# Kernel optimization log

Measured on AMD Instinct MI355X. Metric: run time of the kernel, lower is better.

The kernel has to match this reference:

```python
import jax, jax.numpy as jnp
import numpy as np

ROUTING_ROUNDS = 3
EPS = 1e-9

def squash(s, axis):
    # s * ||s||^2 / (1 + ||s||^2) / ||s||
    sn = jnp.sum(s * s, axis=axis, keepdims=True)
    return s * (sn / (1.0 + sn)) * jax.lax.rsqrt(sn + EPS)

def setup_inputs() -> dict:
    key = jax.random.key(0)
    k1, k2 = jax.random.split(key)
    B, N, D = 32, 2048, 32   # batch, input caps num, input caps dim
    C, V = 64, 32            # output caps num, output caps dim
    input_layer = jax.random.normal(k1, (B, N, D), dtype=jnp.float32)
    W = 0.1 * jax.random.normal(k2, (1, N, C, V, D), dtype=jnp.float32)
    return {"input_layer": input_layer, "W": W}

def reference(input_layer, W):
    # input_layer: [B, N, D]; W: [1, N, C, V, D]
    B, N, D = input_layer.shape
    Wn = W[0]  # [N, C, V, D]
    C, V = Wn.shape[1], Wn.shape[2]
    # caps_predicted (u_hat): [B, N, C, V]  (== tf matmul of W_tiled @ caps_output_tiled, squeezed)
    u_hat = jnp.einsum('bnd,ncvd->bncv', input_layer, Wn)
    b = jnp.zeros((B, N, C), dtype=input_layer.dtype)
    v = None
    for _ in range(ROUTING_ROUNDS):
        r = jax.nn.softmax(b, axis=2)                      # [B, N, C]
        s = jnp.einsum('bnc,bncv->bcv', r, u_hat)          # weighted_sum over input caps
        v = squash(s, axis=-1)                             # [B, C, V]
        # agreement = u_hat^T . v : [B, N, C]
        b = b + jnp.einsum('bncv,bcv->bnc', u_hat, v)
    # match original output shape [B, 1, caps_num, vec_len, 1]
    return v[:, None, :, :, None]
```

## Files before the change

### kernel.cpp

```cpp
#include <hip/hip_runtime.h>
#include <hip/hip_bf16.h>


#define B_ 32
#define N_ 2048
#define D_ 32
#define C_ 64
#define V_ 32

typedef __attribute__((ext_vector_type(4))) float f32x4;
typedef __attribute__((ext_vector_type(4))) int i32x4;
typedef __attribute__((ext_vector_type(2))) int i32x2;
typedef __bf16 bf16x8 __attribute__((ext_vector_type(8)));

__device__ __forceinline__ unsigned f2bf1(float f) {
  unsigned u = __builtin_bit_cast(unsigned, f);
  return (u + 0x7FFFu + ((u >> 16) & 1u)) >> 16;
}
__device__ __forceinline__ float bf2f(unsigned h) {
  unsigned u = h << 16;
  return __builtin_bit_cast(float, u);
}

__device__ __forceinline__ bf16x8 cvt_frag(f32x4 lo, f32x4 hi) {
  i32x4 r;
  r[0] = f2bf1(lo[0]) | (f2bf1(lo[1]) << 16);
  r[1] = f2bf1(lo[2]) | (f2bf1(lo[3]) << 16);
  r[2] = f2bf1(hi[0]) | (f2bf1(hi[1]) << 16);
  r[3] = f2bf1(hi[2]) | (f2bf1(hi[3]) << 16);
  return __builtin_bit_cast(bf16x8, r);
}

__global__ __launch_bounds__(256) void uhat_kernel(const float* __restrict__ x,
                                                   const float* __restrict__ W,
                                                   unsigned short* __restrict__ uh) {
  const int n = blockIdx.x;
  const int wave = threadIdx.x >> 6;
  const int l = threadIdx.x & 63;
  const int l16 = l & 15, kg = l >> 4;

  bf16x8 xb[2];
#pragma unroll
  for (int bt = 0; bt < 2; ++bt) {
    const float* xp = x + (((size_t)(bt * 16 + l16)) * N_ + n) * D_ + kg * 8;
    xb[bt] = cvt_frag(*(const f32x4*)xp, *(const f32x4*)(xp + 4));
  }
  const f32x4 zero = {0.f, 0.f, 0.f, 0.f};
  const float* wbase = W + ((size_t)n * 2048 + wave * 512 + l16) * D_ + kg * 8;
  unsigned short* ubase = uh + (size_t)n * 65536 + (size_t)(wave * 512 + kg * 4);

  f32x4 wl[2][2];
  {
    const float* w0 = wbase;
    const float* w1 = wbase + (size_t)16 * D_;
    wl[0][0] = *(const f32x4*)w0; wl[0][1] = *(const f32x4*)(w0 + 4);
    wl[1][0] = *(const f32x4*)w1; wl[1][1] = *(const f32x4*)(w1 + 4);
  }
#pragma unroll
  for (int pt = 0; pt < 32; ++pt) {
    f32x4 c0 = wl[pt & 1][0], c1 = wl[pt & 1][1];
    if (pt < 30) {
      const float* wp = wbase + (size_t)((pt + 2) * 16) * D_;
      wl[pt & 1][0] = *(const f32x4*)wp;
      wl[pt & 1][1] = *(const f32x4*)(wp + 4);
    }
    bf16x8 wfrag = cvt_frag(c0, c1);
#pragma unroll
    for (int bt = 0; bt < 2; ++bt) {
      f32x4 acc = __builtin_amdgcn_mfma_f32_16x16x32_bf16(wfrag, xb[bt], zero, 0, 0, 0);
      i32x2 dv;
      dv[0] = (int)(f2bf1(acc[0]) | (f2bf1(acc[1]) << 16));
      dv[1] = (int)(f2bf1(acc[2]) | (f2bf1(acc[3]) << 16));
      *(i32x2*)(ubase + (size_t)(bt * 16 + l16) * 2048 + pt * 16) = dv;
    }
  }
}

template <int ROUND>
__global__ __launch_bounds__(256) void routing_kernel(const unsigned short* __restrict__ uh,
                                                      const float* __restrict__ vsum,
                                                      float* __restrict__ part) {
  const int b = blockIdx.x >> 5;
  const int chunk = blockIdx.x & 31;
  const int wave = threadIdx.x >> 6;
  const int l = threadIdx.x & 63;

  float vs[32];
  if (ROUND >= 2) {
    const f32x4* vp = (const f32x4*)(vsum + ((size_t)b * 64 + l) * 32);
#pragma unroll
    for (int i = 0; i < 8; ++i) {
      f32x4 t = vp[i];
      vs[4 * i] = t[0]; vs[4 * i + 1] = t[1]; vs[4 * i + 2] = t[2]; vs[4 * i + 3] = t[3];
    }
  }
  float sacc[32];
#pragma unroll
  for (int v = 0; v < 32; ++v) sacc[v] = 0.f;

  const int n0 = chunk * 64 + wave * 16;
  for (int ni = 0; ni < 16; ++ni) {
    const int n = n0 + ni;
    const i32x4* up = (const i32x4*)(uh + ((size_t)n * 32 + b) * 2048 + l * 32);
    i32x4 qs0 = up[0], qs1 = up[1], qs2 = up[2], qs3 = up[3];
    float u[32];
#pragma unroll
    for (int i = 0; i < 4; ++i) {
      unsigned v0 = (unsigned)qs0[i], v1 = (unsigned)qs1[i], v2 = (unsigned)qs2[i], v3 = (unsigned)qs3[i];
      u[0 + 2 * i] = bf2f(v0 & 0xffffu);  u[0 + 2 * i + 1] = bf2f(v0 >> 16);
      u[8 + 2 * i] = bf2f(v1 & 0xffffu);  u[8 + 2 * i + 1] = bf2f(v1 >> 16);
      u[16 + 2 * i] = bf2f(v2 & 0xffffu); u[16 + 2 * i + 1] = bf2f(v2 >> 16);
      u[24 + 2 * i] = bf2f(v3 & 0xffffu); u[24 + 2 * i + 1] = bf2f(v3 >> 16);
    }
    float r;
    if (ROUND >= 2) {
      float br = 0.f;
#pragma unroll
      for (int v = 0; v < 32; ++v) br = fmaf(u[v], vs[v], br);
      float m = br;
#pragma unroll
      for (int off = 32; off; off >>= 1) m = fmaxf(m, __shfl_xor(m, off, 64));
      float e = __expf(br - m);
      float den = e;
#pragma unroll
      for (int off = 32; off; off >>= 1) den += __shfl_xor(den, off, 64);
      r = e / den;
    } else {
      r = 1.0f / 64.0f;
    }
#pragma unroll
    for (int v = 0; v < 32; ++v) sacc[v] = fmaf(r, u[v], sacc[v]);
  }

  __shared__ float red[4][64][33];
#pragma unroll
  for (int v = 0; v < 32; ++v) red[wave][l][v] = sacc[v];
  __syncthreads();
  const int t = threadIdx.x;
  f32x4 o0, o1;
#pragma unroll
  for (int i = 0; i < 4; ++i) {
    const int e0 = t * 8 + i, e1 = t * 8 + 4 + i;
    o0[i] = red[0][e0 >> 5][e0 & 31] + red[1][e0 >> 5][e0 & 31] +
            red[2][e0 >> 5][e0 & 31] + red[3][e0 >> 5][e0 & 31];
    o1[i] = red[0][e1 >> 5][e1 & 31] + red[1][e1 >> 5][e1 & 31] +
            red[2][e1 >> 5][e1 & 31] + red[3][e1 >> 5][e1 & 31];
  }
  float* pp = part + ((size_t)blockIdx.x) * 2048 + t * 8;
  *(f32x4*)pp = o0;
  *(f32x4*)(pp + 4) = o1;
}

template <int ROUND>
__global__ __launch_bounds__(256) void squash_kernel(const float* __restrict__ part,
                                                     float* __restrict__ vsum,
                                                     float* __restrict__ out) {
  const int t = blockIdx.x * 256 + threadIdx.x;
  const int b = t >> 11;
  const int e = t & 2047;
  float sv = 0.f;
#pragma unroll
  for (int k = 0; k < 32; ++k) sv += part[((size_t)(b * 32 + k)) * 2048 + e];
  float sq = sv * sv;
#pragma unroll
  for (int off = 16; off; off >>= 1) sq += __shfl_xor(sq, off, 64);
  float scale = (sq / (1.f + sq)) * rsqrtf(sq + 1e-9f);
  float val = sv * scale;
  out[t] = val;
  if (ROUND == 1) vsum[t] = val;
  else if (ROUND == 2) vsum[t] += val;
}

extern "C" void kernel_launch(void* const* d_in, const int* in_sizes, int n_in,
                              void* d_out, int out_size, void* d_ws, size_t ws_size,
                              hipStream_t stream) {
  const float* x = (const float*)d_in[0];
  const float* W = (const float*)d_in[1];
  float* out = (float*)d_out;

  const size_t UH_BYTES = (size_t)B_ * N_ * C_ * V_ * 2;
  const size_t PART_BYTES = (size_t)B_ * 32 * 2048 * 4;
  const size_t VSUM_BYTES = (size_t)B_ * C_ * V_ * 4;
  if (ws_size < UH_BYTES + PART_BYTES + VSUM_BYTES) return;

  unsigned short* uh = (unsigned short*)d_ws;
  float* part = (float*)((char*)d_ws + UH_BYTES);
  float* vsum = (float*)((char*)d_ws + UH_BYTES + PART_BYTES);

  uhat_kernel<<<N_, 256, 0, stream>>>(x, W, uh);
  routing_kernel<1><<<B_ * 32, 256, 0, stream>>>(uh, vsum, part);
  squash_kernel<1><<<256, 256, 0, stream>>>(part, vsum, out);
  routing_kernel<2><<<B_ * 32, 256, 0, stream>>>(uh, vsum, part);
  squash_kernel<2><<<256, 256, 0, stream>>>(part, vsum, out);
  routing_kernel<3><<<B_ * 32, 256, 0, stream>>>(uh, vsum, part);
  squash_kernel<3><<<256, 256, 0, stream>>>(part, vsum, out);
}
```

Baseline: 342.9 us.

## Reorder u_hat layout via LDS staging and remap routing blocks to batch pairs

The uhat kernel now stages each group of 8 MFMA output tiles in per-wave LDS and writes u_hat with full 16-byte coalesced stores in a new layout. The layout interleaves batch rows at 16-element granularity inside each n and c-pair. Routing blocks now cover two batches with 32 n each per wave, which halves the grid and changes the partial-sum indexing, and squash is updated to match. The aim is to replace the scattered 8-byte stores in uhat with coalesced ones and to give routing better load locality, at the cost of extra LDS traffic and fewer routing blocks.

```diff
diff --git a/kernel.cpp b/kernel.cpp
--- a/kernel.cpp
+++ b/kernel.cpp
@@ -39,6 +39,9 @@
   const int l = threadIdx.x & 63;
   const int l16 = l & 15, kg = l >> 4;
 
+  __shared__ unsigned short lds[4][8 * 640];
+  unsigned short* wlds = lds[wave];
+
   bf16x8 xb[2];
 #pragma unroll
   for (int bt = 0; bt < 2; ++bt) {
@@ -47,7 +50,7 @@
   }
   const f32x4 zero = {0.f, 0.f, 0.f, 0.f};
   const float* wbase = W + ((size_t)n * 2048 + wave * 512 + l16) * D_ + kg * 8;
-  unsigned short* ubase = uh + (size_t)n * 65536 + (size_t)(wave * 512 + kg * 4);
+  unsigned short* ubase = uh + (((size_t)n * 128 + wave * 32) * 512) + l * 8;
 
   f32x4 wl[2][2];
   {
@@ -56,23 +59,39 @@
     wl[0][0] = *(const f32x4*)w0; wl[0][1] = *(const f32x4*)(w0 + 4);
     wl[1][0] = *(const f32x4*)w1; wl[1][1] = *(const f32x4*)(w1 + 4);
   }
-#pragma unroll
-  for (int pt = 0; pt < 32; ++pt) {
-    f32x4 c0 = wl[pt & 1][0], c1 = wl[pt & 1][1];
-    if (pt < 30) {
-      const float* wp = wbase + (size_t)((pt + 2) * 16) * D_;
-      wl[pt & 1][0] = *(const f32x4*)wp;
-      wl[pt & 1][1] = *(const f32x4*)(wp + 4);
-    }
-    bf16x8 wfrag = cvt_frag(c0, c1);
-#pragma unroll
-    for (int bt = 0; bt < 2; ++bt) {
-      f32x4 acc = __builtin_amdgcn_mfma_f32_16x16x32_bf16(wfrag, xb[bt], zero, 0, 0, 0);
-      i32x2 dv;
-      dv[0] = (int)(f2bf1(acc[0]) | (f2bf1(acc[1]) << 16));
-      dv[1] = (int)(f2bf1(acc[2]) | (f2bf1(acc[3]) << 16));
-      *(i32x2*)(ubase + (size_t)(bt * 16 + l16) * 2048 + pt * 16) = dv;
-    }
+
+#pragma unroll
+  for (int g = 0; g < 4; ++g) {
+#pragma unroll
+    for (int pq = 0; pq < 8; ++pq) {
+      const int pt = g * 8 + pq;
+      f32x4 c0 = wl[pt & 1][0], c1 = wl[pt & 1][1];
+      if (pt < 30) {
+        const float* wp = wbase + (size_t)((pt + 2) * 16) * D_;
+        wl[pt & 1][0] = *(const f32x4*)wp;
+        wl[pt & 1][1] = *(const f32x4*)(wp + 4);
+      }
+      bf16x8 wfrag = cvt_frag(c0, c1);
+#pragma unroll
+      for (int bt = 0; bt < 2; ++bt) {
+        f32x4 acc = __builtin_amdgcn_mfma_f32_16x16x32_bf16(wfrag, xb[bt], zero, 0, 0, 0);
+        i32x2 dv;
+        dv[0] = (int)(f2bf1(acc[0]) | (f2bf1(acc[1]) << 16));
+        dv[1] = (int)(f2bf1(acc[2]) | (f2bf1(acc[3]) << 16));
+        *(i32x2*)(wlds + pq * 640 + (bt * 16 + l16) * 20 + kg * 4) = dv;
+      }
+    }
+    __builtin_amdgcn_sched_barrier(0);
+#pragma unroll
+    for (int k = 0; k < 8; ++k) {
+      const unsigned short* src = wlds + k * 640 + (l >> 1) * 20 + (l & 1) * 8;
+      i32x2 lo = *(const i32x2*)src;
+      i32x2 hi = *(const i32x2*)(src + 4);
+      i32x4 vv;
+      vv[0] = lo[0]; vv[1] = lo[1]; vv[2] = hi[0]; vv[3] = hi[1];
+      *(i32x4*)(ubase + ((size_t)(g * 8 + k)) * 512) = vv;
+    }
+    __builtin_amdgcn_sched_barrier(0);
   }
 }
 
@@ -80,10 +99,12 @@
 __global__ __launch_bounds__(256) void routing_kernel(const unsigned short* __restrict__ uh,
                                                       const float* __restrict__ vsum,
                                                       float* __restrict__ part) {
-  const int b = blockIdx.x >> 5;
+  const int pair = blockIdx.x >> 5;
   const int chunk = blockIdx.x & 31;
-  const int wave = threadIdx.x >> 6;
+  const int w = threadIdx.x >> 6;
   const int l = threadIdx.x & 63;
+  const int b = pair * 2 + (w >> 1);
+  const int n0 = chunk * 64 + (w & 1) * 32;
 
   float vs[32];
   if (ROUND >= 2) {
@@ -98,11 +119,13 @@
 #pragma unroll
   for (int v = 0; v < 32; ++v) sacc[v] = 0.f;
 
-  const int n0 = chunk * 64 + wave * 16;
-  for (int ni = 0; ni < 16; ++ni) {
+  for (int ni = 0; ni < 32; ++ni) {
     const int n = n0 + ni;
-    const i32x4* up = (const i32x4*)(uh + ((size_t)n * 32 + b) * 2048 + l * 32);
-    i32x4 qs0 = up[0], qs1 = up[1], qs2 = up[2], qs3 = up[3];
+    const unsigned short* up = uh + (((size_t)n * 128 + 2 * l) * 32 + b) * 16;
+    i32x4 qs0 = *(const i32x4*)up;
+    i32x4 qs1 = *(const i32x4*)(up + 8);
+    i32x4 qs2 = *(const i32x4*)(up + 512);
+    i32x4 qs3 = *(const i32x4*)(up + 520);
     float u[32];
 #pragma unroll
     for (int i = 0; i < 4; ++i) {
@@ -134,21 +157,24 @@
 
   __shared__ float red[4][64][33];
 #pragma unroll
-  for (int v = 0; v < 32; ++v) red[wave][l][v] = sacc[v];
+  for (int v = 0; v < 32; ++v) red[w][l][v] = sacc[v];
   __syncthreads();
   const int t = threadIdx.x;
-  f32x4 o0, o1;
+  f32x4 o0, o1, p0, p1;
 #pragma unroll
   for (int i = 0; i < 4; ++i) {
     const int e0 = t * 8 + i, e1 = t * 8 + 4 + i;
-    o0[i] = red[0][e0 >> 5][e0 & 31] + red[1][e0 >> 5][e0 & 31] +
-            red[2][e0 >> 5][e0 & 31] + red[3][e0 >> 5][e0 & 31];
-    o1[i] = red[0][e1 >> 5][e1 & 31] + red[1][e1 >> 5][e1 & 31] +
-            red[2][e1 >> 5][e1 & 31] + red[3][e1 >> 5][e1 & 31];
-  }
-  float* pp = part + ((size_t)blockIdx.x) * 2048 + t * 8;
-  *(f32x4*)pp = o0;
-  *(f32x4*)(pp + 4) = o1;
+    o0[i] = red[0][e0 >> 5][e0 & 31] + red[1][e0 >> 5][e0 & 31];
+    o1[i] = red[0][e1 >> 5][e1 & 31] + red[1][e1 >> 5][e1 & 31];
+    p0[i] = red[2][e0 >> 5][e0 & 31] + red[3][e0 >> 5][e0 & 31];
+    p1[i] = red[2][e1 >> 5][e1 & 31] + red[3][e1 >> 5][e1 & 31];
+  }
+  float* pp0 = part + ((size_t)blockIdx.x * 2) * 2048 + t * 8;
+  float* pp1 = part + ((size_t)blockIdx.x * 2 + 1) * 2048 + t * 8;
+  *(f32x4*)pp0 = o0;
+  *(f32x4*)(pp0 + 4) = o1;
+  *(f32x4*)pp1 = p0;
+  *(f32x4*)(pp1 + 4) = p1;
 }
 
 template <int ROUND>
@@ -158,9 +184,11 @@
   const int t = blockIdx.x * 256 + threadIdx.x;
   const int b = t >> 11;
   const int e = t & 2047;
+  const int pr = b >> 1, b01 = b & 1;
   float sv = 0.f;
 #pragma unroll
-  for (int k = 0; k < 32; ++k) sv += part[((size_t)(b * 32 + k)) * 2048 + e];
+  for (int k = 0; k < 32; ++k)
+    sv += part[(((size_t)(pr * 32 + k)) * 2 + b01) * 2048 + e];
   float sq = sv * sv;
 #pragma unroll
   for (int off = 16; off; off >>= 1) sq += __shfl_xor(sq, off, 64);
@@ -179,7 +207,7 @@
   float* out = (float*)d_out;
 
   const size_t UH_BYTES = (size_t)B_ * N_ * C_ * V_ * 2;
-  const size_t PART_BYTES = (size_t)B_ * 32 * 2048 * 4;
+  const size_t PART_BYTES = (size_t)512 * 2 * 2048 * 4;
   const size_t VSUM_BYTES = (size_t)B_ * C_ * V_ * 4;
   if (ws_size < UH_BYTES + PART_BYTES + VSUM_BYTES) return;
 
@@ -188,10 +216,10 @@
   float* vsum = (float*)((char*)d_ws + UH_BYTES + PART_BYTES);
 
   uhat_kernel<<<N_, 256, 0, stream>>>(x, W, uh);
-  routing_kernel<1><<<B_ * 32, 256, 0, stream>>>(uh, vsum, part);
+  routing_kernel<1><<<512, 256, 0, stream>>>(uh, vsum, part);
   squash_kernel<1><<<256, 256, 0, stream>>>(part, vsum, out);
-  routing_kernel<2><<<B_ * 32, 256, 0, stream>>>(uh, vsum, part);
+  routing_kernel<2><<<512, 256, 0, stream>>>(uh, vsum, part);
   squash_kernel<2><<<256, 256, 0, stream>>>(part, vsum, out);
-  routing_kernel<3><<<B_ * 32, 256, 0, stream>>>(uh, vsum, part);
+  routing_kernel<3><<<512, 256, 0, stream>>>(uh, vsum, part);
   squash_kernel<3><<<256, 256, 0, stream>>>(part, vsum, out);
 }
```

Result: slower. 426.4 us (+24.3%).

## Stream W through swizzled LDS double buffer via global_load_lds in uhat kernel

Applied to the files above, without the earlier changes.

The uhat kernel now loads W tiles with direct global-to-LDS loads into a per-wave double buffer, using an XOR swizzle so that LDS reads avoid bank conflicts. Loads for the next phase are issued before the current phase computes, with explicit vmcnt waits. The goal is fuller, more coalesced W streaming, and less register pressure than the earlier register prefetch. The costs are 32 KB of LDS per block, which may cut occupancy, and hand-written waitcnt counts that also count the uh stores, so the synchronisation is fragile.

```diff
diff --git a/kernel.cpp b/kernel.cpp
--- a/kernel.cpp
+++ b/kernel.cpp
@@ -31,6 +31,12 @@
   return __builtin_bit_cast(bf16x8, r);
 }
 
+__device__ __forceinline__ void gload16(const float* g, float* l) {
+  __builtin_amdgcn_global_load_lds(
+      (const __attribute__((address_space(1))) void*)g,
+      (__attribute__((address_space(3))) void*)l, 16, 0, 0);
+}
+
 __global__ __launch_bounds__(256) void uhat_kernel(const float* __restrict__ x,
                                                    const float* __restrict__ W,
                                                    unsigned short* __restrict__ uh) {
@@ -38,6 +44,11 @@
   const int wave = threadIdx.x >> 6;
   const int l = threadIdx.x & 63;
   const int l16 = l & 15, kg = l >> 4;
+  const int lrow = l >> 3, lcol = l & 7;
+
+  __shared__ float lds[4][2][1024];
+  float* wbuf0 = &lds[wave][0][0];
+  float* wbuf1 = &lds[wave][1][0];
 
   bf16x8 xb[2];
 #pragma unroll
@@ -45,33 +56,53 @@
     const float* xp = x + (((size_t)(bt * 16 + l16)) * N_ + n) * D_ + kg * 8;
     xb[bt] = cvt_frag(*(const f32x4*)xp, *(const f32x4*)(xp + 4));
   }
+  __builtin_amdgcn_sched_barrier(0);
+
   const f32x4 zero = {0.f, 0.f, 0.f, 0.f};
-  const float* wbase = W + ((size_t)n * 2048 + wave * 512 + l16) * D_ + kg * 8;
+  const int src_off_f = lrow * 32 + ((((lcol * 16) ^ (lrow << 4))) >> 2);
+  const float* wsrc = W + (size_t)n * 65536 + (size_t)wave * 16384 + src_off_f;
   unsigned short* ubase = uh + (size_t)n * 65536 + (size_t)(wave * 512 + kg * 4);
-
-  f32x4 wl[2][2];
-  {
-    const float* w0 = wbase;
-    const float* w1 = wbase + (size_t)16 * D_;
-    wl[0][0] = *(const f32x4*)w0; wl[0][1] = *(const f32x4*)(w0 + 4);
-    wl[1][0] = *(const f32x4*)w1; wl[1][1] = *(const f32x4*)(w1 + 4);
-  }
-#pragma unroll
-  for (int pt = 0; pt < 32; ++pt) {
-    f32x4 c0 = wl[pt & 1][0], c1 = wl[pt & 1][1];
-    if (pt < 30) {
-      const float* wp = wbase + (size_t)((pt + 2) * 16) * D_;
-      wl[pt & 1][0] = *(const f32x4*)wp;
-      wl[pt & 1][1] = *(const f32x4*)(wp + 4);
-    }
-    bf16x8 wfrag = cvt_frag(c0, c1);
-#pragma unroll
-    for (int bt = 0; bt < 2; ++bt) {
-      f32x4 acc = __builtin_amdgcn_mfma_f32_16x16x32_bf16(wfrag, xb[bt], zero, 0, 0, 0);
-      i32x2 dv;
-      dv[0] = (int)(f2bf1(acc[0]) | (f2bf1(acc[1]) << 16));
-      dv[1] = (int)(f2bf1(acc[2]) | (f2bf1(acc[3]) << 16));
-      *(i32x2*)(ubase + (size_t)(bt * 16 + l16) * 2048 + pt * 16) = dv;
+  const unsigned char* rb0 = (const unsigned char*)wbuf0;
+  const unsigned char* rb1 = (const unsigned char*)wbuf1;
+  const int a_base = (kg * 32) ^ ((l16 & 7) << 4);
+
+#pragma unroll
+  for (int sub = 0; sub < 4; ++sub)
+    gload16(wsrc + sub * 256, wbuf0 + sub * 256);
+
+#pragma unroll
+  for (int ph = 0; ph < 16; ++ph) {
+    if (ph < 15) {
+      const float* ws = wsrc + (size_t)(ph + 1) * 1024;
+      float* dbuf = ((ph + 1) & 1) ? wbuf1 : wbuf0;
+#pragma unroll
+      for (int sub = 0; sub < 4; ++sub)
+        gload16(ws + sub * 256, dbuf + sub * 256);
+    }
+    if (ph == 0) {
+      asm volatile("s_waitcnt vmcnt(4)" ::: "memory");
+    } else if (ph == 15) {
+      asm volatile("s_waitcnt vmcnt(4)" ::: "memory");
+    } else {
+      asm volatile("s_waitcnt vmcnt(8)" ::: "memory");
+    }
+    __builtin_amdgcn_sched_barrier(0);
+    const unsigned char* rb = (ph & 1) ? rb1 : rb0;
+#pragma unroll
+    for (int t = 0; t < 2; ++t) {
+      const int a0 = (t * 16 + l16) * 128 + a_base;
+      f32x4 lo = *(const f32x4*)(rb + a0);
+      f32x4 hi = *(const f32x4*)(rb + (a0 ^ 16));
+      bf16x8 wfrag = cvt_frag(lo, hi);
+      const int pt = ph * 2 + t;
+#pragma unroll
+      for (int bt = 0; bt < 2; ++bt) {
+        f32x4 acc = __builtin_amdgcn_mfma_f32_16x16x32_bf16(wfrag, xb[bt], zero, 0, 0, 0);
+        i32x2 dv;
+        dv[0] = (int)(f2bf1(acc[0]) | (f2bf1(acc[1]) << 16));
+        dv[1] = (int)(f2bf1(acc[2]) | (f2bf1(acc[3]) << 16));
+        *(i32x2*)(ubase + (size_t)(bt * 16 + l16) * 2048 + pt * 16) = dv;
+      }
     }
   }
 }
```

After: 327.2 us. -4.6%, faster.

## Coalesce W loads with bpermute and stage u_hat stores through LDS

Applied to the files above, without the earlier changes.

The u_hat kernel now reads W with fully contiguous per-lane 32-byte loads and uses ds_bpermute to rearrange the values into MFMA fragment order. It also buffers MFMA outputs in a per-wave LDS tile and writes 16-byte coalesced rows to global memory every four steps, replacing scattered 8-byte stores. The goal is better global memory coalescing for the large W read and the u_hat write, at the cost of extra LDS traffic, permute instructions and explicit waits.

```diff
diff --git a/kernel.cpp b/kernel.cpp
--- a/kernel.cpp
+++ b/kernel.cpp
@@ -39,39 +39,63 @@
   const int l = threadIdx.x & 63;
   const int l16 = l & 15, kg = l >> 4;
 
+  __shared__ unsigned short olds[4][32 * 72];
+  unsigned short* obuf = &olds[wave][0];
+
   bf16x8 xb[2];
 #pragma unroll
   for (int bt = 0; bt < 2; ++bt) {
     const float* xp = x + (((size_t)(bt * 16 + l16)) * N_ + n) * D_ + kg * 8;
     xb[bt] = cvt_frag(*(const f32x4*)xp, *(const f32x4*)(xp + 4));
   }
+
   const f32x4 zero = {0.f, 0.f, 0.f, 0.f};
-  const float* wbase = W + ((size_t)n * 2048 + wave * 512 + l16) * D_ + kg * 8;
-  unsigned short* ubase = uh + (size_t)n * 65536 + (size_t)(wave * 512 + kg * 4);
-
-  f32x4 wl[2][2];
-  {
-    const float* w0 = wbase;
-    const float* w1 = wbase + (size_t)16 * D_;
-    wl[0][0] = *(const f32x4*)w0; wl[0][1] = *(const f32x4*)(w0 + 4);
-    wl[1][0] = *(const f32x4*)w1; wl[1][1] = *(const f32x4*)(w1 + 4);
-  }
-#pragma unroll
-  for (int pt = 0; pt < 32; ++pt) {
-    f32x4 c0 = wl[pt & 1][0], c1 = wl[pt & 1][1];
-    if (pt < 30) {
-      const float* wp = wbase + (size_t)((pt + 2) * 16) * D_;
-      wl[pt & 1][0] = *(const f32x4*)wp;
-      wl[pt & 1][1] = *(const f32x4*)(wp + 4);
-    }
-    bf16x8 wfrag = cvt_frag(c0, c1);
+  const float* wsrc = W + (size_t)n * 65536 + (size_t)wave * 16384 + l * 8;
+  unsigned short* ubase = uh + (size_t)n * 65536 + wave * 512;
+  const int bp = ((((l & 15) << 2) | (l >> 4)) << 2);
+
+  f32x4 wa[2], wb[2];
+  wa[0] = *(const f32x4*)(wsrc);
+  wb[0] = *(const f32x4*)(wsrc + 4);
+  wa[1] = *(const f32x4*)(wsrc + 512);
+  wb[1] = *(const f32x4*)(wsrc + 516);
+
+#pragma unroll
+  for (int ph = 0; ph < 32; ++ph) {
+    f32x4 ca = wa[ph & 1], cb = wb[ph & 1];
+    if (ph < 30) {
+      const float* wp = wsrc + (size_t)(ph + 2) * 512;
+      wa[ph & 1] = *(const f32x4*)(wp);
+      wb[ph & 1] = *(const f32x4*)(wp + 4);
+    }
+    i32x4 ia = __builtin_bit_cast(i32x4, ca), ib = __builtin_bit_cast(i32x4, cb);
+    i32x4 oa, ob;
+#pragma unroll
+    for (int j = 0; j < 4; ++j) {
+      oa[j] = __builtin_amdgcn_ds_bpermute(bp, ia[j]);
+      ob[j] = __builtin_amdgcn_ds_bpermute(bp, ib[j]);
+    }
+    bf16x8 wfrag = cvt_frag(__builtin_bit_cast(f32x4, oa), __builtin_bit_cast(f32x4, ob));
 #pragma unroll
     for (int bt = 0; bt < 2; ++bt) {
       f32x4 acc = __builtin_amdgcn_mfma_f32_16x16x32_bf16(wfrag, xb[bt], zero, 0, 0, 0);
       i32x2 dv;
       dv[0] = (int)(f2bf1(acc[0]) | (f2bf1(acc[1]) << 16));
       dv[1] = (int)(f2bf1(acc[2]) | (f2bf1(acc[3]) << 16));
-      *(i32x2*)(ubase + (size_t)(bt * 16 + l16) * 2048 + pt * 16) = dv;
+      *(i32x2*)(obuf + (bt * 16 + l16) * 72 + (ph & 3) * 16 + kg * 4) = dv;
+    }
+    if ((ph & 3) == 3) {
+      asm volatile("s_waitcnt lgkmcnt(0)" ::: "memory");
+      __builtin_amdgcn_sched_barrier(0);
+      const int pbase = (ph >> 2) * 64;
+#pragma unroll
+      for (int i = 0; i < 4; ++i) {
+        const int b = i * 8 + (l >> 3);
+        const unsigned short* s = obuf + b * 72 + (l & 7) * 8;
+        i32x4 v = *(const i32x4*)s;
+        *(i32x4*)(ubase + (size_t)b * 2048 + pbase + (l & 7) * 8) = v;
+      }
+      __builtin_amdgcn_sched_barrier(0);
     }
   }
 }
```

Measured after the change: 306.7 us. -10.6%, faster.
